# Kernel optimization log

Measured on AMD Instinct MI355X. Metric: run time of the kernel, lower is better.

Reference implementation:

```python
import jax, jax.numpy as jnp
import numpy as np

N_NODES = 100_000
N_EDGES = 3_200_000
FAN_IN, FAN_MID, FAN_OUT = 512, 256, 64
NEG_SLOPE = 0.01  # F.leaky_relu default


def setup_inputs() -> dict:
    key = jax.random.key(0)
    ks = jax.random.split(key, 8)
    x = jax.random.normal(ks[0], (N_NODES, FAN_IN), dtype=jnp.float32)
    edge_src = jax.random.randint(ks[1], (N_EDGES,), 0, N_NODES, dtype=jnp.int32)
    edge_dst = jax.random.randint(ks[2], (N_EDGES,), 0, N_NODES, dtype=jnp.int32)
    edge_w1 = jax.random.uniform(ks[3], (N_EDGES,), dtype=jnp.float32)
    edge_w2 = jax.random.uniform(ks[4], (N_EDGES,), dtype=jnp.float32)
    W1 = jax.random.normal(ks[5], (FAN_IN, FAN_MID), dtype=jnp.float32) * (1.0 / np.sqrt(FAN_IN))
    b1 = jnp.zeros((FAN_MID,), dtype=jnp.float32)
    W2 = jax.random.normal(ks[6], (FAN_MID, FAN_OUT), dtype=jnp.float32) * (1.0 / np.sqrt(FAN_MID))
    b2 = jnp.zeros((FAN_OUT,), dtype=jnp.float32)
    return {"x": x, "edge_src": edge_src, "edge_dst": edge_dst,
            "edge_w1": edge_w1, "edge_w2": edge_w2,
            "W1": W1, "b1": b1, "W2": W2, "b2": b2}


def _gcn_layer(x, W, b, src, dst, ew):
    # GraphConvolution: support = x @ W ; out = A @ support + b (A sparse via edges)
    support = x @ W                                 # [N, F_out]
    msgs = support[src] * ew[:, None]               # gather + scale, [E, F_out]
    agg = jax.ops.segment_sum(msgs, dst, num_segments=x.shape[0])  # scatter-add
    return agg + b


def reference(x, edge_src, edge_dst, edge_w1, edge_w2, W1, b1, W2, b2):
    h = _gcn_layer(x, W1, b1, edge_src, edge_dst, edge_w1)
    h = jax.nn.leaky_relu(h, NEG_SLOPE)
    # dropout is identity at inference (training=False)
    h = _gcn_layer(h, W2, b2, edge_src, edge_dst, edge_w2)
    return jax.nn.log_softmax(h, axis=1)
```

## Files before the change

### kernel.cpp

```cpp
#include <hip/hip_runtime.h>
#include <stdint.h>

#define FAN_IN  512
#define FAN_MID 256
#define FAN_OUT 64
#define NEG_SLOPE 0.01f
#define NPB 64
#define CURPAD 16

typedef __bf16 bf16_t;
typedef bf16_t bf16x8 __attribute__((ext_vector_type(8)));
typedef float  f32x4  __attribute__((ext_vector_type(4)));
typedef unsigned short u16x8 __attribute__((ext_vector_type(8)));

__device__ inline unsigned short f2b(float f) {
    union { float f; unsigned int u; } v; v.f = f;
    unsigned int u = v.u;
    return (unsigned short)((u + 0x7fffu + ((u >> 16) & 1u)) >> 16);
}
__device__ inline float b2f(unsigned short u) {
    union { unsigned int u; float f; } v; v.u = ((unsigned int)u) << 16; return v.f;
}

__global__ void zerob_kernel(int* p, int n) {
    int i = blockIdx.x * 256 + threadIdx.x;
    if (i < n) p[i] = 0;
}

__global__ __launch_bounds__(256) void bhist_kernel(const int* __restrict__ dst,
                                                    int* __restrict__ bcount, int E, int nb) {
    __shared__ int lc[2048];
    for (int i = threadIdx.x; i < nb; i += 256) lc[i] = 0;
    __syncthreads();
    int stride = gridDim.x * 256;
    for (int e = blockIdx.x * 256 + threadIdx.x; e < E; e += stride)
        atomicAdd(&lc[dst[e] >> 6], 1);
    __syncthreads();
    for (int i = threadIdx.x; i < nb; i += 256)
        if (lc[i]) atomicAdd(&bcount[i], lc[i]);
}

__global__ void bscan_kernel(const int* __restrict__ bcount, int* __restrict__ boff,
                             int* __restrict__ bcur, int nb, int E) {
    __shared__ int part[1024];
    int t = threadIdx.x;
    int chunk = (nb + 1023) >> 10;
    int s = t * chunk;
    int e = s + chunk; if (e > nb) e = nb;
    int sum = 0;
    for (int i = s; i < e; i++) sum += bcount[i];
    part[t] = sum;
    __syncthreads();
    for (int off = 1; off < 1024; off <<= 1) {
        int v = (t >= off) ? part[t - off] : 0;
        __syncthreads();
        part[t] += v;
        __syncthreads();
    }
    int run = (t == 0) ? 0 : part[t - 1];
    for (int i = s; i < e; i++) {
        boff[i] = run;
        bcur[i * CURPAD] = run;
        run += bcount[i];
    }
    if (t == 1023) boff[nb] = E;
}

__global__ __launch_bounds__(256) void bscatter_kernel(const int* __restrict__ src,
                                                       const int* __restrict__ dst,
                                                       const float* __restrict__ w1,
                                                       const float* __restrict__ w2,
                                                       int* __restrict__ bcur,
                                                       uint4* __restrict__ bstage, int E) {
    int e = blockIdx.x * 256 + threadIdx.x;
    if (e >= E) return;
    int d = dst[e];
    int b = d >> 6;
    int pos = atomicAdd(&bcur[b * CURPAD], 1);
    uint4 v;
    v.x = (unsigned int)src[e];
    v.y = __float_as_uint(w1[e]);
    v.z = __float_as_uint(w2[e]);
    v.w = (unsigned int)d;
    bstage[pos] = v;
}

__global__ __launch_bounds__(256) void bsort_kernel(const uint4* __restrict__ bstage,
                                                    const int* __restrict__ boff,
                                                    int* __restrict__ offsets,
                                                    uint4* __restrict__ csr,
                                                    int Nn, int E, int nb) {
    __shared__ int cnt[NPB];
    __shared__ int scn[NPB];
    __shared__ int cur[NPB];
    int b = blockIdx.x;
    int t = threadIdx.x;
    int base = boff[b], end = boff[b + 1];
    int n0 = b * NPB;
    if (t < NPB) cnt[t] = 0;
    __syncthreads();
    for (int i = base + t; i < end; i += 256)
        atomicAdd(&cnt[bstage[i].w - n0], 1);
    __syncthreads();
    if (t == 0) {
        int run = 0;
        for (int j = 0; j < NPB; j++) { scn[j] = run; run += cnt[j]; }
    }
    __syncthreads();
    if (t < NPB) {
        cur[t] = scn[t];
        int n = n0 + t;
        if (n < Nn) offsets[n] = base + scn[t];
    }
    if (b == nb - 1 && t == 0) offsets[Nn] = E;
    __syncthreads();
    for (int i = base + t; i < end; i += 256) {
        uint4 rec = bstage[i];
        int lp = atomicAdd(&cur[rec.w - n0], 1);
        csr[base + lp] = rec;
    }
}

__global__ void convert_w_kernel(const float* __restrict__ W, unsigned short* __restrict__ Wt,
                                 int K, int N) {
    int idx = blockIdx.x * 256 + threadIdx.x;
    if (idx >= K * N) return;
    int k = idx / N, n = idx % N;
    Wt[(size_t)n * K + k] = f2b(W[idx]);
}

template<int K, int N, bool A_F32>
__global__ __launch_bounds__(256) void gemm_bt(const void* __restrict__ Ap,
                                               const unsigned short* __restrict__ Bt,
                                               unsigned short* __restrict__ C, int M) {
    constexpr int LDT = 40;
    constexpr int NW  = N / 64;
    __shared__ unsigned short As[64 * LDT];
    __shared__ unsigned short Bs[N * LDT];
    const int m0   = blockIdx.x * 64;
    const int tid  = threadIdx.x;
    const int lane = tid & 63;
    const int w    = tid >> 6;
    const int lrow = tid >> 2;
    const int lseg = (tid & 3) * 8;
    const int q    = lane >> 4;
    const int mm   = lane & 15;

    f32x4 acc[4][NW] = {};

    for (int k0 = 0; k0 < K; k0 += 32) {
        __syncthreads();
        {
            int gm = m0 + lrow;
            u16x8 av;
            if (A_F32) {
                const float* A32 = (const float*)Ap;
                if (gm < M) {
                    const float4* pp = (const float4*)(A32 + (size_t)gm * K + k0 + lseg);
                    float4 f0 = pp[0], f1 = pp[1];
                    av[0] = f2b(f0.x); av[1] = f2b(f0.y); av[2] = f2b(f0.z); av[3] = f2b(f0.w);
                    av[4] = f2b(f1.x); av[5] = f2b(f1.y); av[6] = f2b(f1.z); av[7] = f2b(f1.w);
                } else av = (u16x8)0;
            } else {
                const unsigned short* A16 = (const unsigned short*)Ap;
                if (gm < M) av = *(const u16x8*)(A16 + (size_t)gm * K + k0 + lseg);
                else        av = (u16x8)0;
            }
            *(u16x8*)&As[lrow * LDT + lseg] = av;
        }
#pragma unroll
        for (int r = 0; r < N / 64; r++) {
            int nr = r * 64 + lrow;
            *(u16x8*)&Bs[nr * LDT + lseg] =
                *(const u16x8*)(Bt + (size_t)nr * K + k0 + lseg);
        }
        __syncthreads();

        bf16x8 a[4], b[NW];
#pragma unroll
        for (int mi = 0; mi < 4; mi++)
            a[mi] = *(const bf16x8*)&As[(mi * 16 + mm) * LDT + q * 8];
#pragma unroll
        for (int ni = 0; ni < NW; ni++)
            b[ni] = *(const bf16x8*)&Bs[(w * NW * 16 + ni * 16 + mm) * LDT + q * 8];
#pragma unroll
        for (int mi = 0; mi < 4; mi++)
#pragma unroll
            for (int ni = 0; ni < NW; ni++)
                acc[mi][ni] = __builtin_amdgcn_mfma_f32_16x16x32_bf16(a[mi], b[ni], acc[mi][ni], 0, 0, 0);
    }

#pragma unroll
    for (int mi = 0; mi < 4; mi++)
#pragma unroll
        for (int ni = 0; ni < NW; ni++)
#pragma unroll
            for (int r = 0; r < 4; r++) {
                int row = m0 + mi * 16 + q * 4 + r;
                if (row < M)
                    C[(size_t)row * N + w * NW * 16 + ni * 16 + mm] = f2b(acc[mi][ni][r]);
            }
}

__global__ __launch_bounds__(256) void agg1_kernel(const unsigned short* __restrict__ S,
                                                   const int* __restrict__ offsets,
                                                   const uint4* __restrict__ edges,
                                                   const float* __restrict__ b1,
                                                   unsigned short* __restrict__ h, int Nn) {
    int wave = threadIdx.x >> 6;
    int lane = threadIdx.x & 63;
    int node = blockIdx.x * 4 + wave;
    if (node >= Nn) return;
    int s = offsets[node], e = offsets[node + 1];
    float a0 = 0.f, a1 = 0.f, a2 = 0.f, a3 = 0.f;
    int i = s;
    for (; i + 4 <= e; i += 4) {
        uint4 e0 = edges[i], e1 = edges[i + 1], e2 = edges[i + 2], e3 = edges[i + 3];
        ushort4 v0 = *(const ushort4*)(S + (size_t)e0.x * 256 + lane * 4);
        ushort4 v1 = *(const ushort4*)(S + (size_t)e1.x * 256 + lane * 4);
        ushort4 v2 = *(const ushort4*)(S + (size_t)e2.x * 256 + lane * 4);
        ushort4 v3 = *(const ushort4*)(S + (size_t)e3.x * 256 + lane * 4);
        float w0 = __uint_as_float(e0.y), w1 = __uint_as_float(e1.y);
        float w2 = __uint_as_float(e2.y), w3 = __uint_as_float(e3.y);
        a0 += w0 * b2f(v0.x) + w1 * b2f(v1.x) + w2 * b2f(v2.x) + w3 * b2f(v3.x);
        a1 += w0 * b2f(v0.y) + w1 * b2f(v1.y) + w2 * b2f(v2.y) + w3 * b2f(v3.y);
        a2 += w0 * b2f(v0.z) + w1 * b2f(v1.z) + w2 * b2f(v2.z) + w3 * b2f(v3.z);
        a3 += w0 * b2f(v0.w) + w1 * b2f(v1.w) + w2 * b2f(v2.w) + w3 * b2f(v3.w);
    }
    for (; i < e; i++) {
        uint4 ev = edges[i];
        float w = __uint_as_float(ev.y);
        ushort4 v = *(const ushort4*)(S + (size_t)ev.x * 256 + lane * 4);
        a0 += w * b2f(v.x); a1 += w * b2f(v.y); a2 += w * b2f(v.z); a3 += w * b2f(v.w);
    }
    float4 bb = ((const float4*)b1)[lane];
    float r0 = a0 + bb.x, r1 = a1 + bb.y, r2 = a2 + bb.z, r3 = a3 + bb.w;
    r0 = r0 > 0.f ? r0 : r0 * NEG_SLOPE;
    r1 = r1 > 0.f ? r1 : r1 * NEG_SLOPE;
    r2 = r2 > 0.f ? r2 : r2 * NEG_SLOPE;
    r3 = r3 > 0.f ? r3 : r3 * NEG_SLOPE;
    ushort4 o;
    o.x = f2b(r0); o.y = f2b(r1); o.z = f2b(r2); o.w = f2b(r3);
    *(ushort4*)&h[(size_t)node * 256 + lane * 4] = o;
}

__global__ __launch_bounds__(256) void agg2_kernel(const unsigned short* __restrict__ S,
                                                   const int* __restrict__ offsets,
                                                   const uint4* __restrict__ edges,
                                                   const float* __restrict__ b2,
                                                   float* __restrict__ out, int Nn) {
    int wave = threadIdx.x >> 6;
    int lane = threadIdx.x & 63;
    int node = blockIdx.x * 4 + wave;
    if (node >= Nn) return;
    int s = offsets[node], e = offsets[node + 1];
    float acc = 0.f;
    int i = s;
    for (; i + 4 <= e; i += 4) {
        uint4 e0 = edges[i], e1 = edges[i + 1], e2 = edges[i + 2], e3 = edges[i + 3];
        float v0 = b2f(S[(size_t)e0.x * 64 + lane]);
        float v1 = b2f(S[(size_t)e1.x * 64 + lane]);
        float v2 = b2f(S[(size_t)e2.x * 64 + lane]);
        float v3 = b2f(S[(size_t)e3.x * 64 + lane]);
        acc += __uint_as_float(e0.z) * v0 + __uint_as_float(e1.z) * v1
             + __uint_as_float(e2.z) * v2 + __uint_as_float(e3.z) * v3;
    }
    for (; i < e; i++) {
        uint4 ev = edges[i];
        acc += __uint_as_float(ev.z) * b2f(S[(size_t)ev.x * 64 + lane]);
    }
    float logit = acc + b2[lane];
    float m = logit;
    for (int off = 32; off; off >>= 1) m = fmaxf(m, __shfl_xor(m, off));
    float ex = expf(logit - m);
    float sum = ex;
    for (int off = 32; off; off >>= 1) sum += __shfl_xor(sum, off);
    out[(size_t)node * 64 + lane] = logit - m - logf(sum);
}

extern "C" void kernel_launch(void* const* d_in, const int* in_sizes, int n_in,
                              void* d_out, int out_size, void* d_ws, size_t ws_size,
                              hipStream_t stream) {
    const float* x    = (const float*)d_in[0];
    const int*   esrc = (const int*)d_in[1];
    const int*   edst = (const int*)d_in[2];
    const float* ew1  = (const float*)d_in[3];
    const float* ew2  = (const float*)d_in[4];
    const float* W1   = (const float*)d_in[5];
    const float* b1   = (const float*)d_in[6];
    const float* W2   = (const float*)d_in[7];
    const float* b2   = (const float*)d_in[8];
    float* out = (float*)d_out;
    const int Nn = in_sizes[0] / FAN_IN;
    const int E  = in_sizes[1];
    const int NB = (Nn + NPB - 1) / NPB;

    char* p = (char*)d_ws;
    auto alloc = [&](size_t bytes) -> char* {
        char* r = p;
        p += (bytes + 255) & ~(size_t)255;
        return r;
    };
    size_t s1_bytes = (size_t)Nn * FAN_MID * 2;
    size_t st_bytes = (size_t)E * 16;
    char* s1_region = alloc(s1_bytes > st_bytes ? s1_bytes : st_bytes);
    unsigned short* support1 = (unsigned short*)s1_region;
    uint4*          bstage   = (uint4*)s1_region;
    unsigned short* h        = (unsigned short*)alloc((size_t)Nn * FAN_MID * 2);
    unsigned short* support2 = (unsigned short*)alloc((size_t)Nn * FAN_OUT * 2);
    unsigned short* W1t      = (unsigned short*)alloc((size_t)FAN_IN * FAN_MID * 2);
    unsigned short* W2t      = (unsigned short*)alloc((size_t)FAN_MID * FAN_OUT * 2);
    int*            bcount   = (int*)alloc((size_t)NB * 4);
    int*            boff     = (int*)alloc(((size_t)NB + 1) * 4);
    int*            bcur     = (int*)alloc((size_t)NB * CURPAD * 4);
    int*            offsets  = (int*)alloc(((size_t)Nn + 1) * 4);
    uint4*          csr      = (uint4*)alloc((size_t)E * 16);

    zerob_kernel<<<(NB + 255) / 256, 256, 0, stream>>>(bcount, NB);
    bhist_kernel<<<512, 256, 0, stream>>>(edst, bcount, E, NB);
    bscan_kernel<<<1, 1024, 0, stream>>>(bcount, boff, bcur, NB, E);
    bscatter_kernel<<<(E + 255) / 256, 256, 0, stream>>>(esrc, edst, ew1, ew2, bcur, bstage, E);
    bsort_kernel<<<NB, 256, 0, stream>>>(bstage, boff, offsets, csr, Nn, E, NB);

    convert_w_kernel<<<(FAN_IN * FAN_MID + 255) / 256, 256, 0, stream>>>(W1, W1t, FAN_IN, FAN_MID);
    convert_w_kernel<<<(FAN_MID * FAN_OUT + 255) / 256, 256, 0, stream>>>(W2, W2t, FAN_MID, FAN_OUT);

    gemm_bt<FAN_IN, FAN_MID, true><<<dim3((Nn + 63) / 64, 1), 256, 0, stream>>>(
        x, W1t, support1, Nn);
    agg1_kernel<<<(Nn + 3) / 4, 256, 0, stream>>>(support1, offsets, csr, b1, h, Nn);

    gemm_bt<FAN_MID, FAN_OUT, false><<<dim3((Nn + 63) / 64, 1), 256, 0, stream>>>(
        h, W2t, support2, Nn);
    agg2_kernel<<<(Nn + 3) / 4, 256, 0, stream>>>(support2, offsets, csr, b2, out, Nn);
}
```

Before: 985.2 us.

## Replace global-atomic bucket scatter with per-block partitioned counting sort

Edge bucketing now splits the edges into 256 contiguous chunks. Each chunk builds a local histogram in LDS, a per-bucket scan turns those into exclusive write bases, and the scatter then claims positions with LDS atomics instead of contended global atomics on padded counters. The bucket width grows from 64 to 128 nodes, which halves the bucket count so it fits the 1024-entry shared arrays. The cost is an extra scan kernel, extra workspace for the per-chunk count and base tables, and fewer, larger blocks in the scatter phase, which may limit parallelism.

Result: faster. 865.2 us (-12.2%).

```diff
diff --git a/kernel.cpp b/kernel.cpp
--- a/kernel.cpp
+++ b/kernel.cpp
@@ -5,8 +5,9 @@
 #define FAN_MID 256
 #define FAN_OUT 64
 #define NEG_SLOPE 0.01f
-#define NPB 64
-#define CURPAD 16
+#define NPB 128
+#define MAXNB 1024
+#define BPART 256
 
 typedef __bf16 bf16_t;
 typedef bf16_t bf16x8 __attribute__((ext_vector_type(8)));
@@ -27,21 +28,28 @@
     if (i < n) p[i] = 0;
 }
 
-__global__ __launch_bounds__(256) void bhist_kernel(const int* __restrict__ dst,
-                                                    int* __restrict__ bcount, int E, int nb) {
-    __shared__ int lc[2048];
+__global__ __launch_bounds__(256) void part_hist(const int* __restrict__ dst,
+                                                 int* __restrict__ gcount,
+                                                 int* __restrict__ bcount,
+                                                 int E, int nb, int chunk) {
+    __shared__ int lc[MAXNB];
+    int blk = blockIdx.x;
     for (int i = threadIdx.x; i < nb; i += 256) lc[i] = 0;
     __syncthreads();
-    int stride = gridDim.x * 256;
-    for (int e = blockIdx.x * 256 + threadIdx.x; e < E; e += stride)
-        atomicAdd(&lc[dst[e] >> 6], 1);
-    __syncthreads();
-    for (int i = threadIdx.x; i < nb; i += 256)
-        if (lc[i]) atomicAdd(&bcount[i], lc[i]);
+    int s = blk * chunk;
+    int e = s + chunk; if (e > E) e = E;
+    for (int i = s + threadIdx.x; i < e; i += 256)
+        atomicAdd(&lc[dst[i] >> 7], 1);
+    __syncthreads();
+    for (int i = threadIdx.x; i < nb; i += 256) {
+        int c = lc[i];
+        gcount[blk * nb + i] = c;
+        if (c) atomicAdd(&bcount[i], c);
+    }
 }
 
 __global__ void bscan_kernel(const int* __restrict__ bcount, int* __restrict__ boff,
-                             int* __restrict__ bcur, int nb, int E) {
+                             int nb, int E) {
     __shared__ int part[1024];
     int t = threadIdx.x;
     int chunk = (nb + 1023) >> 10;
@@ -60,29 +68,52 @@
     int run = (t == 0) ? 0 : part[t - 1];
     for (int i = s; i < e; i++) {
         boff[i] = run;
-        bcur[i * CURPAD] = run;
         run += bcount[i];
     }
     if (t == 1023) boff[nb] = E;
 }
 
-__global__ __launch_bounds__(256) void bscatter_kernel(const int* __restrict__ src,
-                                                       const int* __restrict__ dst,
-                                                       const float* __restrict__ w1,
-                                                       const float* __restrict__ w2,
-                                                       int* __restrict__ bcur,
-                                                       uint4* __restrict__ bstage, int E) {
-    int e = blockIdx.x * 256 + threadIdx.x;
-    if (e >= E) return;
-    int d = dst[e];
-    int b = d >> 6;
-    int pos = atomicAdd(&bcur[b * CURPAD], 1);
-    uint4 v;
-    v.x = (unsigned int)src[e];
-    v.y = __float_as_uint(w1[e]);
-    v.z = __float_as_uint(w2[e]);
-    v.w = (unsigned int)d;
-    bstage[pos] = v;
+__global__ __launch_bounds__(BPART) void part_scan(const int* __restrict__ gcount,
+                                                   const int* __restrict__ boff,
+                                                   int* __restrict__ gbase, int nb) {
+    __shared__ int v[BPART];
+    int bucket = blockIdx.x;
+    int t = threadIdx.x;
+    int val = gcount[t * nb + bucket];
+    v[t] = val;
+    __syncthreads();
+    for (int off = 1; off < BPART; off <<= 1) {
+        int x = (t >= off) ? v[t - off] : 0;
+        __syncthreads();
+        v[t] += x;
+        __syncthreads();
+    }
+    gbase[t * nb + bucket] = (t == 0 ? 0 : v[t - 1]) + boff[bucket];
+}
+
+__global__ __launch_bounds__(256) void part_scatter(const int* __restrict__ src,
+                                                    const int* __restrict__ dst,
+                                                    const float* __restrict__ w1,
+                                                    const float* __restrict__ w2,
+                                                    const int* __restrict__ gbase,
+                                                    uint4* __restrict__ bstage,
+                                                    int E, int nb, int chunk) {
+    __shared__ int lcur[MAXNB];
+    int blk = blockIdx.x;
+    for (int i = threadIdx.x; i < nb; i += 256) lcur[i] = gbase[blk * nb + i];
+    __syncthreads();
+    int s = blk * chunk;
+    int e = s + chunk; if (e > E) e = E;
+    for (int i = s + threadIdx.x; i < e; i += 256) {
+        int d = dst[i];
+        int pos = atomicAdd(&lcur[d >> 7], 1);
+        uint4 v;
+        v.x = (unsigned int)src[i];
+        v.y = __float_as_uint(w1[i]);
+        v.z = __float_as_uint(w2[i]);
+        v.w = (unsigned int)d;
+        bstage[pos] = v;
+    }
 }
 
 __global__ __launch_bounds__(256) void bsort_kernel(const uint4* __restrict__ bstage,
@@ -294,6 +325,7 @@
     const int Nn = in_sizes[0] / FAN_IN;
     const int E  = in_sizes[1];
     const int NB = (Nn + NPB - 1) / NPB;
+    const int chunk = (E + BPART - 1) / BPART;
 
     char* p = (char*)d_ws;
     auto alloc = [&](size_t bytes) -> char* {
@@ -312,14 +344,16 @@
     unsigned short* W2t      = (unsigned short*)alloc((size_t)FAN_MID * FAN_OUT * 2);
     int*            bcount   = (int*)alloc((size_t)NB * 4);
     int*            boff     = (int*)alloc(((size_t)NB + 1) * 4);
-    int*            bcur     = (int*)alloc((size_t)NB * CURPAD * 4);
+    int*            gcount   = (int*)alloc((size_t)BPART * NB * 4);
+    int*            gbase    = (int*)alloc((size_t)BPART * NB * 4);
     int*            offsets  = (int*)alloc(((size_t)Nn + 1) * 4);
     uint4*          csr      = (uint4*)alloc((size_t)E * 16);
 
     zerob_kernel<<<(NB + 255) / 256, 256, 0, stream>>>(bcount, NB);
-    bhist_kernel<<<512, 256, 0, stream>>>(edst, bcount, E, NB);
-    bscan_kernel<<<1, 1024, 0, stream>>>(bcount, boff, bcur, NB, E);
-    bscatter_kernel<<<(E + 255) / 256, 256, 0, stream>>>(esrc, edst, ew1, ew2, bcur, bstage, E);
+    part_hist<<<BPART, 256, 0, stream>>>(edst, gcount, bcount, E, NB, chunk);
+    bscan_kernel<<<1, 1024, 0, stream>>>(bcount, boff, NB, E);
+    part_scan<<<NB, BPART, 0, stream>>>(gcount, boff, gbase, NB);
+    part_scatter<<<BPART, 256, 0, stream>>>(esrc, edst, ew1, ew2, gbase, bstage, E, NB, chunk);
     bsort_kernel<<<NB, 256, 0, stream>>>(bstage, boff, offsets, csr, Nn, E, NB);
 
     convert_w_kernel<<<(FAN_IN * FAN_MID + 255) / 256, 256, 0, stream>>>(W1, W1t, FAN_IN, FAN_MID);
```
